# Optimization experiments

Measured on AMD Instinct MI355X. Metric: run time of the kernel, lower is better.

## Reference

```python
import jax, jax.numpy as jnp
import numpy as np

KERNEL_MUL = 2.0
KERNEL_NUM = 5

def setup_inputs() -> dict:
    key = jax.random.key(0)
    k1, k2 = jax.random.split(key)
    source = jax.random.normal(k1, (4096, 256), dtype=jnp.float32)
    target = jax.random.normal(k2, (4096, 256), dtype=jnp.float32)
    return {"source": source, "target": target}

def reference(source, target):
    B = source.shape[0]
    total = jnp.concatenate([source, target], axis=0)           # [2N, D]
    n = total.shape[0]
    # pairwise squared L2 distances via expansion (same math as
    # ((total0 - total1)**2).sum(2) without the [2N,2N,D] intermediate)
    sq = jnp.sum(total * total, axis=-1)                         # [2N]
    l2 = jnp.maximum(sq[:, None] + sq[None, :] - 2.0 * (total @ total.T), 0.0)  # [2N,2N]
    # bandwidth from data mean of off-diagonal distances (detached in torch via .data)
    bandwidth = jax.lax.stop_gradient(jnp.sum(l2)) / (n * n - n)
    bandwidth = bandwidth / (KERNEL_MUL ** (KERNEL_NUM // 2))
    kernels = jnp.zeros_like(l2)
    for i in range(KERNEL_NUM):
        kernels = kernels + jnp.exp(-l2 / (bandwidth * (KERNEL_MUL ** i)))
    xx = kernels[:B, :B]
    yy = kernels[B:, B:]
    xy = kernels[:B, B:]
    yx = kernels[B:, :B]
    return jnp.mean(xx + yy - xy - yx)
```

## Files before the change

kernel.cpp:

```cpp
#include <hip/hip_runtime.h>


#define NROWS 8192
#define BHALF 4096
#define DDIM  256
#define TILE  128
#define BK    32
#define NTILE 64
#define NBLK  2080

typedef __attribute__((ext_vector_type(8))) short bf16x8;
typedef __attribute__((ext_vector_type(4))) float f32x4;
typedef __attribute__((ext_vector_type(2))) float f32x2;
typedef __attribute__((ext_vector_type(4))) unsigned short u16x4;

struct Ws {
  float coef;
  float Spart[256];
  float cpart[256][256];
  float sq[NROWS];
  float part[NBLK];
};

__device__ __forceinline__ unsigned short f2bf(float x) {
  unsigned int u = __builtin_bit_cast(unsigned int, x);
  return (unsigned short)((u + 0x7fffu + ((u >> 16) & 1u)) >> 16);
}

__device__ __forceinline__ const float* row_ptr(const float* src, const float* tgt, int i) {
  return (i < BHALF) ? (src + (size_t)i * DDIM) : (tgt + (size_t)(i - BHALF) * DDIM);
}

__global__ __launch_bounds__(256) void k_prep(const float* __restrict__ src,
                                              const float* __restrict__ tgt,
                                              Ws* __restrict__ ws,
                                              unsigned short* __restrict__ tb,
                                              int conv) {
  __shared__ float cls[4][256];
  __shared__ float sred[4];
  int tid = threadIdx.x, wave = tid >> 6, lane = tid & 63;
  int row0 = blockIdx.x * 32 + wave * 8;
  float c0 = 0.f, c1 = 0.f, c2 = 0.f, c3 = 0.f;
  float s[8];
  #pragma unroll
  for (int r = 0; r < 8; ++r) {
    const float4* rp = (const float4*)row_ptr(src, tgt, row0 + r);
    float4 x = rp[lane];
    if (conv) {
      u16x4 b = { f2bf(x.x), f2bf(x.y), f2bf(x.z), f2bf(x.w) };
      *(u16x4*)&tb[(size_t)(row0 + r) * DDIM + lane * 4] = b;
    }
    c0 += x.x; c1 += x.y; c2 += x.z; c3 += x.w;
    s[r] = x.x * x.x + x.y * x.y + x.z * x.z + x.w * x.w;
  }
  #pragma unroll
  for (int off = 32; off > 0; off >>= 1) {
    #pragma unroll
    for (int r = 0; r < 8; ++r) s[r] += __shfl_xor(s[r], off);
  }
  if (lane == 0) {
    float Sw = 0.f;
    #pragma unroll
    for (int r = 0; r < 8; ++r) { ws->sq[row0 + r] = s[r]; Sw += s[r]; }
    sred[wave] = Sw;
  }
  cls[wave][lane * 4 + 0] = c0;
  cls[wave][lane * 4 + 1] = c1;
  cls[wave][lane * 4 + 2] = c2;
  cls[wave][lane * 4 + 3] = c3;
  __syncthreads();
  ws->cpart[blockIdx.x][tid] = cls[0][tid] + cls[1][tid] + cls[2][tid] + cls[3][tid];
  if (tid == 0) ws->Spart[blockIdx.x] = sred[0] + sred[1] + sred[2] + sred[3];
}

__global__ __launch_bounds__(256) void k_bw(Ws* __restrict__ ws) {
  __shared__ float redm[4], reds[4];
  int tid = threadIdx.x, wave = tid >> 6, lane = tid & 63;
  float mc = 0.f;
  for (int b0 = 0; b0 < 256; b0 += 16) {
    float v[16];
    #pragma unroll
    for (int j = 0; j < 16; ++j) v[j] = ws->cpart[b0 + j][tid];
    #pragma unroll
    for (int j = 0; j < 16; ++j) mc += v[j];
  }
  float p = mc * mc;
  float sp = ws->Spart[tid];
  #pragma unroll
  for (int off = 32; off > 0; off >>= 1) {
    p  += __shfl_xor(p, off);
    sp += __shfl_xor(sp, off);
  }
  if (lane == 0) { redm[wave] = p; reds[wave] = sp; }
  __syncthreads();
  if (tid == 0) {
    float msq = redm[0] + redm[1] + redm[2] + redm[3];
    float S   = reds[0] + reds[1] + reds[2] + reds[3];
    double n = (double)NROWS;
    double sum_l2 = 2.0 * n * (double)S - 2.0 * (double)msq;
    double bw = sum_l2 / (n * n - n) / 4.0;
    ws->coef = (float)(1.4426950408889634 / (16.0 * bw));
  }
}

__device__ __forceinline__ void stage32(const unsigned short* gA,
                                        const unsigned short* gB,
                                        unsigned short* lA, unsigned short* lB,
                                        int kcs) {
  #pragma unroll
  for (int t = 0; t < 2; ++t) {
    __builtin_amdgcn_global_load_lds(
        (const __attribute__((address_space(1))) void*)(gA + (size_t)(t * 16) * DDIM + kcs * BK),
        (__attribute__((address_space(3))) void*)(lA + (t * 16) * BK), 16, 0, 0);
    __builtin_amdgcn_global_load_lds(
        (const __attribute__((address_space(1))) void*)(gB + (size_t)(t * 16) * DDIM + kcs * BK),
        (__attribute__((address_space(3))) void*)(lB + (t * 16) * BK), 16, 0, 0);
  }
}

template <int FAST>
__global__ __launch_bounds__(256, 4) void k_main(const unsigned short* __restrict__ tb,
                                                 const float* __restrict__ src,
                                                 const float* __restrict__ tgt,
                                                 Ws* __restrict__ ws) {
  int bid = blockIdx.x;
  int idx = (bid & 7) * (NBLK / 8) + (bid >> 3);
  int ti = (int)((129.0 - sqrt(129.0 * 129.0 - 8.0 * (double)idx)) * 0.5);
  while (64 * (ti + 1) - ((ti + 1) * ti) / 2 <= idx) ++ti;
  while (64 * ti - (ti * (ti - 1)) / 2 > idx) --ti;
  int tj = ti + (idx - (64 * ti - (ti * (ti - 1)) / 2));

  __shared__ __align__(16) unsigned short As[2][TILE * BK];
  __shared__ __align__(16) unsigned short Bs[2][TILE * BK];
  __shared__ float wsum[4];

  int tid = threadIdx.x;
  int wave = tid >> 6, lane = tid & 63;
  int wm = wave >> 1, wn = wave & 1;
  int lr = lane & 15, q = lane >> 4;
  int Ib = ti * TILE, Jb = tj * TILE;

  f32x4 zero = {0.f, 0.f, 0.f, 0.f};
  f32x4 acc[4][4];
  #pragma unroll
  for (int m = 0; m < 4; ++m)
    #pragma unroll
    for (int n = 0; n < 4; ++n) acc[m][n] = zero;

  const int coff = ((q ^ ((lr >> 1) & 3)) << 3);

  if (FAST) {
    int lrow = lane >> 2;
    int lchk = (lane & 3) ^ ((lane >> 3) & 3);
    const unsigned short* gA = tb + (size_t)(Ib + wave * 32 + lrow) * DDIM + lchk * 8;
    const unsigned short* gB = tb + (size_t)(Jb + wave * 32 + lrow) * DDIM + lchk * 8;
    unsigned short* lA0 = &As[0][wave * 32 * BK];
    unsigned short* lB0 = &Bs[0][wave * 32 * BK];
    unsigned short* lA1 = &As[1][wave * 32 * BK];
    unsigned short* lB1 = &Bs[1][wave * 32 * BK];

    stage32(gA, gB, lA0, lB0, 0);
    __syncthreads();
    #pragma unroll
    for (int kcs = 0; kcs < 8; ++kcs) {
      if (kcs < 7)
        stage32(gA, gB, ((kcs + 1) & 1) ? lA1 : lA0,
                        ((kcs + 1) & 1) ? lB1 : lB0, kcs + 1);
      const unsigned short* Ab = As[kcs & 1];
      const unsigned short* Bb = Bs[kcs & 1];
      bf16x8 af[4], bfr[4];
      #pragma unroll
      for (int m = 0; m < 4; ++m)
        af[m] = *(const bf16x8*)&Ab[(wm * 64 + m * 16 + lr) * BK + coff];
      #pragma unroll
      for (int n = 0; n < 4; ++n)
        bfr[n] = *(const bf16x8*)&Bb[(wn * 64 + n * 16 + lr) * BK + coff];
      #pragma unroll
      for (int m = 0; m < 4; ++m)
        #pragma unroll
        for (int n = 0; n < 4; ++n)
          acc[m][n] = __builtin_amdgcn_mfma_f32_16x16x32_bf16(af[m], bfr[n], acc[m][n], 0, 0, 0);
      if (kcs < 7) __syncthreads();
    }
  } else {
    int row = tid >> 1, h = tid & 1;
    int fsw = (row >> 1) & 3;
    const float4* rpA = (const float4*)row_ptr(src, tgt, Ib + row);
    const float4* rpB = (const float4*)row_ptr(src, tgt, Jb + row);
    #pragma unroll
    for (int kcs = 0; kcs < 8; ++kcs) {
      if (kcs) __syncthreads();
      unsigned short* lA = As[kcs & 1];
      unsigned short* lB = Bs[kcs & 1];
      #pragma unroll
      for (int cc = 0; cc < 2; ++cc) {
        int c = h * 2 + cc;
        int slot = c ^ fsw;
        float4 v0 = rpA[kcs * 8 + c * 2], v1 = rpA[kcs * 8 + c * 2 + 1];
        u16x4 a0 = { f2bf(v0.x), f2bf(v0.y), f2bf(v0.z), f2bf(v0.w) };
        u16x4 a1 = { f2bf(v1.x), f2bf(v1.y), f2bf(v1.z), f2bf(v1.w) };
        *(u16x4*)&lA[row * BK + slot * 8]     = a0;
        *(u16x4*)&lA[row * BK + slot * 8 + 4] = a1;
        float4 w0 = rpB[kcs * 8 + c * 2], w1 = rpB[kcs * 8 + c * 2 + 1];
        u16x4 b0 = { f2bf(w0.x), f2bf(w0.y), f2bf(w0.z), f2bf(w0.w) };
        u16x4 b1 = { f2bf(w1.x), f2bf(w1.y), f2bf(w1.z), f2bf(w1.w) };
        *(u16x4*)&lB[row * BK + slot * 8]     = b0;
        *(u16x4*)&lB[row * BK + slot * 8 + 4] = b1;
      }
      __syncthreads();
      const unsigned short* Ab = As[kcs & 1];
      const unsigned short* Bb = Bs[kcs & 1];
      bf16x8 af[4], bfr[4];
      #pragma unroll
      for (int m = 0; m < 4; ++m)
        af[m] = *(const bf16x8*)&Ab[(wm * 64 + m * 16 + lr) * BK + coff];
      #pragma unroll
      for (int n = 0; n < 4; ++n)
        bfr[n] = *(const bf16x8*)&Bb[(wn * 64 + n * 16 + lr) * BK + coff];
      #pragma unroll
      for (int m = 0; m < 4; ++m)
        #pragma unroll
        for (int n = 0; n < 4; ++n)
          acc[m][n] = __builtin_amdgcn_mfma_f32_16x16x32_bf16(af[m], bfr[n], acc[m][n], 0, 0, 0);
    }
  }

  float coef = ws->coef;
  float coef2 = 2.f * coef;
  int ibase = Ib + wm * 64;
  int jbase = Jb + wn * 64;
  float nscj[4];
  f32x2 nsci01[4], nsci23[4];
  #pragma unroll
  for (int n = 0; n < 4; ++n) nscj[n] = -ws->sq[jbase + n * 16 + lr] * coef;
  #pragma unroll
  for (int m = 0; m < 4; ++m) {
    nsci01[m] = f32x2{ -ws->sq[ibase + m * 16 + q * 4 + 0] * coef,
                       -ws->sq[ibase + m * 16 + q * 4 + 1] * coef };
    nsci23[m] = f32x2{ -ws->sq[ibase + m * 16 + q * 4 + 2] * coef,
                       -ws->sq[ibase + m * 16 + q * 4 + 3] * coef };
  }

  const f32x2 c2v = { coef2, coef2 };
  f32x2 accA = {0.f, 0.f}, accB = {0.f, 0.f};
  f32x2 accC = {0.f, 0.f}, accD = {0.f, 0.f};
  #pragma unroll
  for (int m = 0; m < 4; ++m) {
    #pragma unroll
    for (int n = 0; n < 4; ++n) {
      f32x4 g = acc[m][n];
      f32x2 bj = { nscj[n], nscj[n] };
      f32x2 b01 = nsci01[m] + bj;
      f32x2 b23 = nsci23[m] + bj;
      f32x2 a01 = f32x2{g[0], g[1]} * c2v + b01;
      f32x2 a23 = f32x2{g[2], g[3]} * c2v + b23;
      f32x2 t0, t1;
      t0.x = __builtin_amdgcn_exp2f(a01.x); t0.y = __builtin_amdgcn_exp2f(a01.y);
      t1.x = __builtin_amdgcn_exp2f(a23.x); t1.y = __builtin_amdgcn_exp2f(a23.y);
      f32x2 p0 = t0 * t0, p1 = t1 * t1;
      f32x2 q0 = p0 * p0, q1 = p1 * p1;
      f32x2 r0v = q0 * q0, r1v = q1 * q1;
      accA += t0 + p0;
      accB += q0 + r0v;
      accA = r0v * r0v + accA;
      accC += t1 + p1;
      accD += q1 + r1v;
      accC = r1v * r1v + accC;
    }
  }
  float lsum = (accA.x + accA.y) + (accB.x + accB.y)
             + (accC.x + accC.y) + (accD.x + accD.y);
  #pragma unroll
  for (int off = 32; off > 0; off >>= 1) lsum += __shfl_xor(lsum, off);
  if (lane == 0) wsum[wave] = lsum;
  __syncthreads();
  if (tid == 0) {
    float tot = wsum[0] + wsum[1] + wsum[2] + wsum[3];
    float sA = (ti < 32) ? 1.f : -1.f;
    float sB = (tj < 32) ? 1.f : -1.f;
    float fac = sA * sB * ((ti == tj) ? 1.f : 2.f);
    ws->part[blockIdx.x] = fac * tot;
  }
}

__global__ __launch_bounds__(256) void k_final(const Ws* __restrict__ ws,
                                               float* __restrict__ out) {
  __shared__ double red[4];
  int tid = threadIdx.x, wave = tid >> 6, lane = tid & 63;
  double s = 0.0;
  for (int i = tid; i < NBLK; i += 256) s += (double)ws->part[i];
  #pragma unroll
  for (int off = 32; off > 0; off >>= 1) s += __shfl_xor(s, off);
  if (lane == 0) red[wave] = s;
  __syncthreads();
  if (tid == 0)
    out[0] = (float)((red[0] + red[1] + red[2] + red[3]) /
                     ((double)BHALF * (double)BHALF));
}

extern "C" void kernel_launch(void* const* d_in, const int* in_sizes, int n_in,
                              void* d_out, int out_size, void* d_ws, size_t ws_size,
                              hipStream_t stream) {
  const float* src = (const float*)d_in[0];
  const float* tgt = (const float*)d_in[1];
  Ws* ws = (Ws*)d_ws;
  float* out = (float*)d_out;

  size_t wsoff = (sizeof(Ws) + 255) & ~(size_t)255;
  size_t need = wsoff + (size_t)NROWS * DDIM * 2;
  bool fast = ws_size >= need;
  unsigned short* tb = fast ? (unsigned short*)((char*)d_ws + wsoff) : nullptr;

  hipLaunchKernelGGL(k_prep, dim3(256), dim3(256), 0, stream, src, tgt, ws, tb,
                     fast ? 1 : 0);
  hipLaunchKernelGGL(k_bw, dim3(1), dim3(256), 0, stream, ws);
  if (fast)
    hipLaunchKernelGGL((k_main<1>), dim3(NBLK), dim3(256), 0, stream, tb, src, tgt, ws);
  else
    hipLaunchKernelGGL((k_main<0>), dim3(NBLK), dim3(256), 0, stream, tb, src, tgt, ws);
  hipLaunchKernelGGL(k_final, dim3(1), dim3(256), 0, stream, ws, out);
}
```

Before: 102.0 us.

## Pre-tile bf16 buffer into swizzled LDS-image layout and overlap prefetch with partial waitcnt

The prep kernel now writes the bf16 copy in a tiled layout: each 128-row by 32-column chunk sits contiguously, already carrying the LDS XOR swizzle. The main kernel can then issue fully contiguous 16-byte global_load_lds per lane. The full __syncthreads before each MFMA stage is replaced by s_waitcnt vmcnt(4) plus a raw s_barrier, so the next stage's prefetch stays in flight while the current tile is consumed. This aims to cut global-load address overhead and the stalls from draining every outstanding load each iteration. It depends on hand-counted vmcnt values and raw barriers being correct.

Measured after the change: 101.5 us. About the same (-0.5%).

```diff
diff --git a/kernel.cpp b/kernel.cpp
--- a/kernel.cpp
+++ b/kernel.cpp
@@ -48,7 +48,12 @@
     float4 x = rp[lane];
     if (conv) {
       u16x4 b = { f2bf(x.x), f2bf(x.y), f2bf(x.z), f2bf(x.w) };
-      *(u16x4*)&tb[(size_t)(row0 + r) * DDIM + lane * 4] = b;
+      int rg = row0 + r;
+      int t = rg >> 7, rl = rg & 127;
+      int cg = lane >> 1;
+      int k8 = cg >> 2, cwp = cg & 3;
+      int slot = cwp ^ ((rl >> 1) & 3);
+      *(u16x4*)&tb[((size_t)(t * 8 + k8) * 128 + rl) * 32 + slot * 8 + (lane & 1) * 4] = b;
     }
     c0 += x.x; c1 += x.y; c2 += x.z; c3 += x.w;
     s[r] = x.x * x.x + x.y * x.y + x.z * x.z + x.w * x.w;
@@ -110,11 +115,11 @@
   #pragma unroll
   for (int t = 0; t < 2; ++t) {
     __builtin_amdgcn_global_load_lds(
-        (const __attribute__((address_space(1))) void*)(gA + (size_t)(t * 16) * DDIM + kcs * BK),
-        (__attribute__((address_space(3))) void*)(lA + (t * 16) * BK), 16, 0, 0);
+        (const __attribute__((address_space(1))) void*)(gA + (size_t)kcs * 4096 + t * 512),
+        (__attribute__((address_space(3))) void*)(lA + t * 512), 16, 0, 0);
     __builtin_amdgcn_global_load_lds(
-        (const __attribute__((address_space(1))) void*)(gB + (size_t)(t * 16) * DDIM + kcs * BK),
-        (__attribute__((address_space(3))) void*)(lB + (t * 16) * BK), 16, 0, 0);
+        (const __attribute__((address_space(1))) void*)(gB + (size_t)kcs * 4096 + t * 512),
+        (__attribute__((address_space(3))) void*)(lB + t * 512), 16, 0, 0);
   }
 }
 
@@ -150,22 +155,24 @@
   const int coff = ((q ^ ((lr >> 1) & 3)) << 3);
 
   if (FAST) {
-    int lrow = lane >> 2;
-    int lchk = (lane & 3) ^ ((lane >> 3) & 3);
-    const unsigned short* gA = tb + (size_t)(Ib + wave * 32 + lrow) * DDIM + lchk * 8;
-    const unsigned short* gB = tb + (size_t)(Jb + wave * 32 + lrow) * DDIM + lchk * 8;
-    unsigned short* lA0 = &As[0][wave * 32 * BK];
-    unsigned short* lB0 = &Bs[0][wave * 32 * BK];
-    unsigned short* lA1 = &As[1][wave * 32 * BK];
-    unsigned short* lB1 = &Bs[1][wave * 32 * BK];
+    const unsigned short* gA = tb + (size_t)ti * 32768 + wave * 1024 + lane * 8;
+    const unsigned short* gB = tb + (size_t)tj * 32768 + wave * 1024 + lane * 8;
+    unsigned short* lA0 = &As[0][wave * 1024];
+    unsigned short* lB0 = &Bs[0][wave * 1024];
+    unsigned short* lA1 = &As[1][wave * 1024];
+    unsigned short* lB1 = &Bs[1][wave * 1024];
 
     stage32(gA, gB, lA0, lB0, 0);
-    __syncthreads();
     #pragma unroll
     for (int kcs = 0; kcs < 8; ++kcs) {
-      if (kcs < 7)
+      if (kcs < 7) {
         stage32(gA, gB, ((kcs + 1) & 1) ? lA1 : lA0,
                         ((kcs + 1) & 1) ? lB1 : lB0, kcs + 1);
+        asm volatile("s_waitcnt vmcnt(4)" ::: "memory");
+      } else {
+        asm volatile("s_waitcnt vmcnt(0)" ::: "memory");
+      }
+      __builtin_amdgcn_s_barrier();
       const unsigned short* Ab = As[kcs & 1];
       const unsigned short* Bb = Bs[kcs & 1];
       bf16x8 af[4], bfr[4];
@@ -180,7 +187,7 @@
         #pragma unroll
         for (int n = 0; n < 4; ++n)
           acc[m][n] = __builtin_amdgcn_mfma_f32_16x16x32_bf16(af[m], bfr[n], acc[m][n], 0, 0, 0);
-      if (kcs < 7) __syncthreads();
+      __builtin_amdgcn_s_barrier();
     }
   } else {
     int row = tid >> 1, h = tid & 1;
```
